# Kernel optimization log

Hardware: AMD Instinct MI355X
Metric: run time of the kernel (lower is better)

## Reference

```python
import jax, jax.numpy as jnp
import numpy as np

B, S, I, H, O = 64, 2048, 128, 256, 128


def setup_inputs() -> dict:
    key = jax.random.key(0)
    ks = jax.random.split(key, 7)
    s = 1.0 / np.sqrt(H)
    return {
        "x": jax.random.normal(ks[0], (B, S, I), dtype=jnp.float32),
        "W_ih": jax.random.uniform(ks[1], (H, I), jnp.float32, -s, s),
        "W_hh": jax.random.uniform(ks[2], (H, H), jnp.float32, -s, s),
        "b_ih": jax.random.uniform(ks[3], (H,), jnp.float32, -s, s),
        "b_hh": jax.random.uniform(ks[4], (H,), jnp.float32, -s, s),
        "W_fc": jax.random.uniform(ks[5], (O, H), jnp.float32, -s, s),
        "b_fc": jax.random.uniform(ks[6], (O,), jnp.float32, -s, s),
    }


def reference(x, W_ih, W_hh, b_ih, b_hh, W_fc, b_fc):
    # h_t = tanh(x_t @ W_ih^T + h_{t-1} @ W_hh^T + b_ih + b_hh)
    b = b_ih + b_hh
    # Precompute input projection for all timesteps in one GEMM: [B,S,H]
    xproj = jnp.einsum('bsi,hi->bsh', x, W_ih) + b

    def step(h, xp_t):  # h: [B,H], xp_t: [B,H]
        h_next = jnp.tanh(xp_t + h @ W_hh.T)
        return h_next, h_next

    h0 = jnp.zeros((B, H), dtype=x.dtype)
    _, hs = jax.lax.scan(step, h0, jnp.swapaxes(xproj, 0, 1))  # hs: [S,B,H]
    hidden_states = jnp.swapaxes(hs, 0, 1)  # [B,S,H]
    outputs = jnp.einsum('bsh,oh->bso', hidden_states, W_fc) + b_fc  # [B,S,O]
    return outputs, hidden_states
```

## Files before the change

### kernel.cpp

```cpp
#include <hip/hip_runtime.h>

#define BB 64
#define SS 2048
#define II 128
#define HH 256
#define OO 128

__global__ void prep_kernel(const float* __restrict__ W_ih, const float* __restrict__ b_ih,
                            const float* __restrict__ b_hh, const float* __restrict__ W_fc,
                            float* __restrict__ wihT, float* __restrict__ wfcT,
                            float* __restrict__ biasc) {
    int idx = blockIdx.x * 256 + threadIdx.x;
    if (idx < HH * II) {
        int j = idx / II, k = idx % II;
        wihT[k * HH + j] = W_ih[idx];
    }
    if (idx < OO * HH) {
        int j = idx / HH, k = idx % HH;
        wfcT[k * OO + j] = W_fc[idx];
    }
    if (idx < HH) biasc[idx] = b_ih[idx] + b_hh[idx];
}

template<int KD, int JD, int RT>
__global__ __launch_bounds__(256, 2)
void gemm_rk(const float* __restrict__ A, const float* __restrict__ Wt,
             const float* __restrict__ bias, float* __restrict__ C) {
    constexpr int KT = 64;
    constexpr int TJ = JD / 8;
    constexpr int TR = RT / 8;
    static_assert(TJ * TR == 256, "bad tiling");

    __shared__ __align__(16) float a_lds[RT][KT];
    __shared__ __align__(16) float w_lds[KT][JD];

    const int tid = threadIdx.x;
    const int tj = tid % TJ;
    const int tr = tid / TJ;
    const long r0 = (long)blockIdx.x * RT;

    float acc[8][8];
#pragma unroll
    for (int r = 0; r < 8; ++r)
#pragma unroll
        for (int j = 0; j < 8; ++j) acc[r][j] = 0.0f;

    for (int kt = 0; kt < KD; kt += KT) {
        {
            constexpr int NF4 = RT * KT / 4;
#pragma unroll
            for (int f = 0; f < NF4 / 256; ++f) {
                int fl = f * 256 + tid;
                int rr = fl / (KT / 4), kk4 = fl % (KT / 4);
                *(float4*)&a_lds[rr][kk4 * 4] =
                    *(const float4*)&A[(r0 + rr) * KD + kt + kk4 * 4];
            }
        }
        {
            constexpr int NF4 = KT * JD / 4;
#pragma unroll
            for (int f = 0; f < NF4 / 256; ++f) {
                int fl = f * 256 + tid;
                int kk = fl / (JD / 4), jj4 = fl % (JD / 4);
                *(float4*)&w_lds[kk][jj4 * 4] =
                    *(const float4*)&Wt[(long)(kt + kk) * JD + jj4 * 4];
            }
        }
        __syncthreads();

#pragma unroll 4
        for (int k4 = 0; k4 < KT; k4 += 4) {
            float4 xv[8];
#pragma unroll
            for (int r = 0; r < 8; ++r)
                xv[r] = *(const float4*)&a_lds[tr * 8 + r][k4];
#pragma unroll
            for (int i = 0; i < 4; ++i) {
                float4 wa = *(const float4*)&w_lds[k4 + i][tj * 8];
                float4 wb = *(const float4*)&w_lds[k4 + i][tj * 8 + 4];
#pragma unroll
                for (int r = 0; r < 8; ++r) {
                    float xs = (i == 0) ? xv[r].x : (i == 1) ? xv[r].y
                             : (i == 2) ? xv[r].z : xv[r].w;
                    acc[r][0] = fmaf(xs, wa.x, acc[r][0]);
                    acc[r][1] = fmaf(xs, wa.y, acc[r][1]);
                    acc[r][2] = fmaf(xs, wa.z, acc[r][2]);
                    acc[r][3] = fmaf(xs, wa.w, acc[r][3]);
                    acc[r][4] = fmaf(xs, wb.x, acc[r][4]);
                    acc[r][5] = fmaf(xs, wb.y, acc[r][5]);
                    acc[r][6] = fmaf(xs, wb.z, acc[r][6]);
                    acc[r][7] = fmaf(xs, wb.w, acc[r][7]);
                }
            }
        }
        __syncthreads();
    }

    float4 b0 = *(const float4*)&bias[tj * 8];
    float4 b1 = *(const float4*)&bias[tj * 8 + 4];
#pragma unroll
    for (int r = 0; r < 8; ++r) {
        long row = r0 + tr * 8 + r;
        float4 o0, o1;
        o0.x = acc[r][0] + b0.x; o0.y = acc[r][1] + b0.y;
        o0.z = acc[r][2] + b0.z; o0.w = acc[r][3] + b0.w;
        o1.x = acc[r][4] + b1.x; o1.y = acc[r][5] + b1.y;
        o1.z = acc[r][6] + b1.z; o1.w = acc[r][7] + b1.w;
        *(float4*)&C[row * JD + tj * 8]     = o0;
        *(float4*)&C[row * JD + tj * 8 + 4] = o1;
    }
}

__global__ __launch_bounds__(512, 2)
void rnn_scan(const float* __restrict__ W_hh, float* __restrict__ hid) {
    const int b = blockIdx.x;
    const int tid = threadIdx.x;
    const int og = tid & 63;
    const int kg = tid >> 6;

    __shared__ __align__(16) float h_lds[HH];
    __shared__ __align__(16) float part[8][HH];

    float4 w[4][8];
#pragma unroll
    for (int g = 0; g < 4; ++g)
#pragma unroll
        for (int i4 = 0; i4 < 8; ++i4)
            w[g][i4] = *(const float4*)&W_hh[(og * 4 + g) * HH + kg * 32 + i4 * 4];

    if (tid < HH) h_lds[tid] = 0.0f;

    float* __restrict__ base = hid + (size_t)b * SS * HH;
    float xp0 = 0.0f, xp1 = 0.0f;
    if (tid < HH) { xp0 = base[tid]; xp1 = base[HH + tid]; }
    __syncthreads();

#pragma unroll 1
    for (int t = 0; t < SS; ++t) {
        float xp2 = 0.0f;
        if (tid < HH && t + 2 < SS) xp2 = base[(size_t)(t + 2) * HH + tid];

        const float4* hp = (const float4*)&h_lds[kg * 32];
        float acc[4] = {0.f, 0.f, 0.f, 0.f};
#pragma unroll
        for (int i4 = 0; i4 < 8; ++i4) {
            float4 hv = hp[i4];
#pragma unroll
            for (int g = 0; g < 4; ++g) {
                acc[g] = fmaf(hv.x, w[g][i4].x, acc[g]);
                acc[g] = fmaf(hv.y, w[g][i4].y, acc[g]);
                acc[g] = fmaf(hv.z, w[g][i4].z, acc[g]);
                acc[g] = fmaf(hv.w, w[g][i4].w, acc[g]);
            }
        }
        *(float4*)&part[kg][og * 4] = make_float4(acc[0], acc[1], acc[2], acc[3]);
        __syncthreads();

        if (tid < HH) {
            float s = xp0;
#pragma unroll
            for (int q = 0; q < 8; ++q) s += part[q][tid];
            float cx = fminf(fmaxf(s, -15.0f), 15.0f);
            float e = __expf(2.0f * cx);
            float hn = (e - 1.0f) / (e + 1.0f);
            h_lds[tid] = hn;
            base[(size_t)t * HH + tid] = hn;
        }
        __syncthreads();
        xp0 = xp1; xp1 = xp2;
    }
}

extern "C" void kernel_launch(void* const* d_in, const int* in_sizes, int n_in,
                              void* d_out, int out_size, void* d_ws, size_t ws_size,
                              hipStream_t stream) {
    const float* x    = (const float*)d_in[0];
    const float* W_ih = (const float*)d_in[1];
    const float* W_hh = (const float*)d_in[2];
    const float* b_ih = (const float*)d_in[3];
    const float* b_hh = (const float*)d_in[4];
    const float* W_fc = (const float*)d_in[5];
    const float* b_fc = (const float*)d_in[6];

    float* out_fc  = (float*)d_out;
    float* hidden  = (float*)d_out + (size_t)BB * SS * OO;

    float* wihT  = (float*)d_ws;
    float* wfcT  = wihT + II * HH;
    float* biasc = wfcT + HH * OO;

    const long NR = (long)BB * SS;

    prep_kernel<<<128, 256, 0, stream>>>(W_ih, b_ih, b_hh, W_fc, wihT, wfcT, biasc);

    gemm_rk<II, HH, 64><<<NR / 64, 256, 0, stream>>>(x, wihT, biasc, hidden);

    rnn_scan<<<BB, 512, 0, stream>>>(W_hh, hidden);

    gemm_rk<HH, OO, 128><<<NR / 128, 256, 0, stream>>>(hidden, wfcT, b_fc, out_fc);
}
```

Measured before the change: 1.626 ms.

## Reduce RNN scan partial sums with wave shuffles and double-buffered hidden state

The recurrent scan kernel is restructured so each wavefront owns 32 output rows. Within a wave, lanes split the K dimension four ways and combine their partial dot products with xor shuffles instead of a shared-memory partial buffer. The hidden state is double-buffered in padded LDS, which drops one of the two block barriers per timestep. Each thread now keeps 128 weight floats in registers, which raises register pressure, and only a quarter of the lanes do the tanh and the stores.

```diff
diff --git a/kernel.cpp b/kernel.cpp
--- a/kernel.cpp
+++ b/kernel.cpp
@@ -113,61 +113,87 @@
 
 __global__ __launch_bounds__(512, 2)
 void rnn_scan(const float* __restrict__ W_hh, float* __restrict__ hid) {
-    const int b = blockIdx.x;
+    const int b   = blockIdx.x;
     const int tid = threadIdx.x;
-    const int og = tid & 63;
-    const int kg = tid >> 6;
-
-    __shared__ __align__(16) float h_lds[HH];
-    __shared__ __align__(16) float part[8][HH];
-
-    float4 w[4][8];
-#pragma unroll
-    for (int g = 0; g < 4; ++g)
-#pragma unroll
-        for (int i4 = 0; i4 < 8; ++i4)
-            w[g][i4] = *(const float4*)&W_hh[(og * 4 + g) * HH + kg * 32 + i4 * 4];
-
-    if (tid < HH) h_lds[tid] = 0.0f;
+    const int w   = tid >> 6;
+    const int l   = tid & 63;
+    const int sl  = l & 15;
+    const int q   = l >> 4;
+
+    const int j0 = w * 32 + sl * 2;
+    const int k0 = q * 64;
+
+    __shared__ __align__(16) float h_lds[2][4 * 68];
+
+    float4 wA[16], wB[16];
+#pragma unroll
+    for (int i = 0; i < 16; ++i) {
+        wA[i] = *(const float4*)&W_hh[(size_t)j0 * HH + k0 + i * 4];
+        wB[i] = *(const float4*)&W_hh[(size_t)(j0 + 1) * HH + k0 + i * 4];
+    }
+
+    for (int i = tid; i < 2 * 4 * 68; i += 512) ((float*)h_lds)[i] = 0.0f;
 
     float* __restrict__ base = hid + (size_t)b * SS * HH;
-    float xp0 = 0.0f, xp1 = 0.0f;
-    if (tid < HH) { xp0 = base[tid]; xp1 = base[HH + tid]; }
+    float2 xp0 = make_float2(0.f, 0.f), xp1 = xp0;
+    if (q == 0) {
+        xp0 = *(const float2*)&base[j0];
+        xp1 = *(const float2*)&base[HH + j0];
+    }
     __syncthreads();
 
 #pragma unroll 1
     for (int t = 0; t < SS; ++t) {
-        float xp2 = 0.0f;
-        if (tid < HH && t + 2 < SS) xp2 = base[(size_t)(t + 2) * HH + tid];
-
-        const float4* hp = (const float4*)&h_lds[kg * 32];
-        float acc[4] = {0.f, 0.f, 0.f, 0.f};
-#pragma unroll
-        for (int i4 = 0; i4 < 8; ++i4) {
-            float4 hv = hp[i4];
-#pragma unroll
-            for (int g = 0; g < 4; ++g) {
-                acc[g] = fmaf(hv.x, w[g][i4].x, acc[g]);
-                acc[g] = fmaf(hv.y, w[g][i4].y, acc[g]);
-                acc[g] = fmaf(hv.z, w[g][i4].z, acc[g]);
-                acc[g] = fmaf(hv.w, w[g][i4].w, acc[g]);
-            }
-        }
-        *(float4*)&part[kg][og * 4] = make_float4(acc[0], acc[1], acc[2], acc[3]);
+        float2 xp2 = make_float2(0.f, 0.f);
+        if (q == 0 && t + 2 < SS)
+            xp2 = *(const float2*)&base[(size_t)(t + 2) * HH + j0];
+
+        const float4* hb = (const float4*)&h_lds[t & 1][q * 68];
+        float a0 = 0.f, a1 = 0.f, c0 = 0.f, c1 = 0.f;
+#pragma unroll
+        for (int i = 0; i < 16; i += 2) {
+            float4 h0 = hb[i];
+            float4 h1 = hb[i + 1];
+            a0 = fmaf(h0.x, wA[i].x, a0);
+            a0 = fmaf(h0.y, wA[i].y, a0);
+            a0 = fmaf(h0.z, wA[i].z, a0);
+            a0 = fmaf(h0.w, wA[i].w, a0);
+            a1 = fmaf(h1.x, wA[i + 1].x, a1);
+            a1 = fmaf(h1.y, wA[i + 1].y, a1);
+            a1 = fmaf(h1.z, wA[i + 1].z, a1);
+            a1 = fmaf(h1.w, wA[i + 1].w, a1);
+            c0 = fmaf(h0.x, wB[i].x, c0);
+            c0 = fmaf(h0.y, wB[i].y, c0);
+            c0 = fmaf(h0.z, wB[i].z, c0);
+            c0 = fmaf(h0.w, wB[i].w, c0);
+            c1 = fmaf(h1.x, wB[i + 1].x, c1);
+            c1 = fmaf(h1.y, wB[i + 1].y, c1);
+            c1 = fmaf(h1.z, wB[i + 1].z, c1);
+            c1 = fmaf(h1.w, wB[i + 1].w, c1);
+        }
+        float sA = a0 + a1;
+        float sB = c0 + c1;
+        sA += __shfl_xor(sA, 16, 64);
+        sA += __shfl_xor(sA, 32, 64);
+        sB += __shfl_xor(sB, 16, 64);
+        sB += __shfl_xor(sB, 32, 64);
+
+        if (q == 0) {
+            float s0 = xp0.x + sA;
+            float s1 = xp0.y + sB;
+            s0 = fminf(fmaxf(s0, -15.0f), 15.0f);
+            s1 = fminf(fmaxf(s1, -15.0f), 15.0f);
+            float e0 = __expf(2.0f * s0);
+            float e1 = __expf(2.0f * s1);
+            float hn0 = (e0 - 1.0f) / (e0 + 1.0f);
+            float hn1 = (e1 - 1.0f) / (e1 + 1.0f);
+            int qq = j0 >> 6, ii = j0 & 63;
+            *(float2*)&h_lds[(t & 1) ^ 1][qq * 68 + ii] = make_float2(hn0, hn1);
+            *(float2*)&base[(size_t)t * HH + j0] = make_float2(hn0, hn1);
+        }
         __syncthreads();
-
-        if (tid < HH) {
-            float s = xp0;
-#pragma unroll
-            for (int q = 0; q < 8; ++q) s += part[q][tid];
-            float cx = fminf(fmaxf(s, -15.0f), 15.0f);
-            float e = __expf(2.0f * cx);
-            float hn = (e - 1.0f) / (e + 1.0f);
-            h_lds[tid] = hn;
-            base[(size_t)t * HH + tid] = hn;
-        }
-        __syncthreads();
-        xp0 = xp1; xp1 = xp2;
+        xp0 = xp1;
+        xp1 = xp2;
     }
 }
 
@@ -192,10 +218,7 @@
     const long NR = (long)BB * SS;
 
     prep_kernel<<<128, 256, 0, stream>>>(W_ih, b_ih, b_hh, W_fc, wihT, wfcT, biasc);
-
     gemm_rk<II, HH, 64><<<NR / 64, 256, 0, stream>>>(x, wihT, biasc, hidden);
-
     rnn_scan<<<BB, 512, 0, stream>>>(W_hh, hidden);
-
     gemm_rk<HH, OO, 128><<<NR / 128, 256, 0, stream>>>(hidden, wfcT, b_fc, out_fc);
 }
```

After: 1.770 ms. 1.09x slower.

## Restructure RNN scan with warp-shuffle reduction and double-buffered hidden state

Applied to the files above, without the earlier changes.

The recurrent scan now uses 1024 threads per batch row. Each output unit is handled by 4 lanes of one wavefront, and the partial dot products are combined with cross-lane shuffles instead of an LDS partial-sum array. The hidden state is double-buffered in padded LDS, so each timestep needs one barrier instead of two. Tanh is computed with a cheaper fdividef form and the clamp is removed. This shortens the serial per-step critical path but raises thread count and register pressure, and large inputs now rely on expf overflow behaving well.

```diff
diff --git a/kernel.cpp b/kernel.cpp
--- a/kernel.cpp
+++ b/kernel.cpp
@@ -111,63 +111,76 @@
     }
 }
 
-__global__ __launch_bounds__(512, 2)
+__global__ __launch_bounds__(1024, 4)
 void rnn_scan(const float* __restrict__ W_hh, float* __restrict__ hid) {
-    const int b = blockIdx.x;
+    const int b   = blockIdx.x;
     const int tid = threadIdx.x;
-    const int og = tid & 63;
-    const int kg = tid >> 6;
-
-    __shared__ __align__(16) float h_lds[HH];
-    __shared__ __align__(16) float part[8][HH];
-
-    float4 w[4][8];
-#pragma unroll
-    for (int g = 0; g < 4; ++g)
-#pragma unroll
-        for (int i4 = 0; i4 < 8; ++i4)
-            w[g][i4] = *(const float4*)&W_hh[(og * 4 + g) * HH + kg * 32 + i4 * 4];
-
-    if (tid < HH) h_lds[tid] = 0.0f;
+    const int w   = tid >> 6;
+    const int l   = tid & 63;
+    const int sl  = l & 15;
+    const int q   = l >> 4;
+
+    const int j  = w * 16 + sl;
+    const int k0 = q * 64;
+
+    __shared__ __align__(16) float h_lds[2][4 * 68];
+
+    float4 wv[16];
+#pragma unroll
+    for (int i = 0; i < 16; ++i)
+        wv[i] = *(const float4*)&W_hh[(size_t)j * HH + k0 + i * 4];
+#pragma unroll
+    for (int i = 0; i < 16; ++i)
+        asm volatile("" : "+v"(wv[i].x), "+v"(wv[i].y), "+v"(wv[i].z), "+v"(wv[i].w));
+
+    for (int i = tid; i < 2 * 4 * 68; i += 1024) ((float*)h_lds)[i] = 0.0f;
 
     float* __restrict__ base = hid + (size_t)b * SS * HH;
-    float xp0 = 0.0f, xp1 = 0.0f;
-    if (tid < HH) { xp0 = base[tid]; xp1 = base[HH + tid]; }
+    float xp0 = base[j];
+    float xp1 = base[HH + j];
     __syncthreads();
 
 #pragma unroll 1
     for (int t = 0; t < SS; ++t) {
-        float xp2 = 0.0f;
-        if (tid < HH && t + 2 < SS) xp2 = base[(size_t)(t + 2) * HH + tid];
-
-        const float4* hp = (const float4*)&h_lds[kg * 32];
-        float acc[4] = {0.f, 0.f, 0.f, 0.f};
-#pragma unroll
-        for (int i4 = 0; i4 < 8; ++i4) {
-            float4 hv = hp[i4];
-#pragma unroll
-            for (int g = 0; g < 4; ++g) {
-                acc[g] = fmaf(hv.x, w[g][i4].x, acc[g]);
-                acc[g] = fmaf(hv.y, w[g][i4].y, acc[g]);
-                acc[g] = fmaf(hv.z, w[g][i4].z, acc[g]);
-                acc[g] = fmaf(hv.w, w[g][i4].w, acc[g]);
-            }
-        }
-        *(float4*)&part[kg][og * 4] = make_float4(acc[0], acc[1], acc[2], acc[3]);
+        float xp2 = (t + 2 < SS) ? base[(size_t)(t + 2) * HH + j] : 0.0f;
+
+        const float4* hb = (const float4*)&h_lds[t & 1][q * 68];
+        float a0 = 0.f, a1 = 0.f, a2 = 0.f, a3 = 0.f;
+#pragma unroll
+        for (int i = 0; i < 16; i += 4) {
+            float4 h0 = hb[i], h1 = hb[i + 1], h2 = hb[i + 2], h3 = hb[i + 3];
+            a0 = fmaf(h0.x, wv[i].x, a0);
+            a0 = fmaf(h0.y, wv[i].y, a0);
+            a0 = fmaf(h0.z, wv[i].z, a0);
+            a0 = fmaf(h0.w, wv[i].w, a0);
+            a1 = fmaf(h1.x, wv[i + 1].x, a1);
+            a1 = fmaf(h1.y, wv[i + 1].y, a1);
+            a1 = fmaf(h1.z, wv[i + 1].z, a1);
+            a1 = fmaf(h1.w, wv[i + 1].w, a1);
+            a2 = fmaf(h2.x, wv[i + 2].x, a2);
+            a2 = fmaf(h2.y, wv[i + 2].y, a2);
+            a2 = fmaf(h2.z, wv[i + 2].z, a2);
+            a2 = fmaf(h2.w, wv[i + 2].w, a2);
+            a3 = fmaf(h3.x, wv[i + 3].x, a3);
+            a3 = fmaf(h3.y, wv[i + 3].y, a3);
+            a3 = fmaf(h3.z, wv[i + 3].z, a3);
+            a3 = fmaf(h3.w, wv[i + 3].w, a3);
+        }
+        float s = (a0 + a1) + (a2 + a3);
+        s += __shfl_xor(s, 16, 64);
+        s += __shfl_xor(s, 32, 64);
+        s += xp0;
+
+        float e  = __expf(2.0f * s);
+        float hn = 1.0f - __fdividef(2.0f, e + 1.0f);
+
+        if (q == 0) {
+            h_lds[(t & 1) ^ 1][(j >> 6) * 68 + (j & 63)] = hn;
+            base[(size_t)t * HH + j] = hn;
+        }
         __syncthreads();
-
-        if (tid < HH) {
-            float s = xp0;
-#pragma unroll
-            for (int q = 0; q < 8; ++q) s += part[q][tid];
-            float cx = fminf(fmaxf(s, -15.0f), 15.0f);
-            float e = __expf(2.0f * cx);
-            float hn = (e - 1.0f) / (e + 1.0f);
-            h_lds[tid] = hn;
-            base[(size_t)t * HH + tid] = hn;
-        }
-        __syncthreads();
-        xp0 = xp1; xp1 = xp2;
+        xp0 = xp1;
+        xp1 = xp2;
     }
 }
 
@@ -192,10 +205,7 @@
     const long NR = (long)BB * SS;
 
     prep_kernel<<<128, 256, 0, stream>>>(W_ih, b_ih, b_hh, W_fc, wihT, wfcT, biasc);
-
     gemm_rk<II, HH, 64><<<NR / 64, 256, 0, stream>>>(x, wihT, biasc, hidden);
-
-    rnn_scan<<<BB, 512, 0, stream>>>(W_hh, hidden);
-
+    rnn_scan<<<BB, 1024, 0, stream>>>(W_hh, hidden);
     gemm_rk<HH, OO, 128><<<NR / 128, 256, 0, stream>>>(hidden, wfcT, b_fc, out_fc);
 }
```

Measured after the change: 1.848 ms. +13.6%, slower.
